# Optimization experiments

Measured on AMD Instinct MI355X. Metric: run time of the kernel, lower is better.

Reference implementation:

```python
import jax, jax.numpy as jnp
from jax import lax
import numpy as np

DIM = 384
H = W = 32
B = 32
HALF = DIM // 2


def _parc(x, pe, w, b, axis):
    """Global circular depthwise conv along `axis` (2=H, 3=W). w: (C,1,kh,kw)."""
    x = x + pe
    k = x.shape[axis]
    if axis == 2:
        x_cat = jnp.concatenate([x, x[:, :, : k - 1, :]], axis=2)
    else:
        x_cat = jnp.concatenate([x, x[:, :, :, : k - 1]], axis=3)
    out = lax.conv_general_dilated(
        x_cat, w, window_strides=(1, 1), padding='VALID',
        dimension_numbers=('NCHW', 'OIHW', 'NCHW'),
        feature_group_count=x.shape[1])
    return out + b[None, :, None, None]


def setup_inputs() -> dict:
    key = jax.random.key(0)
    ks = jax.random.split(key, 12)
    std = 0.02
    return {
        'x': jax.random.normal(ks[0], (B, DIM, H, W), jnp.float32),
        'pe_h': std * jax.random.normal(ks[1], (1, HALF, H, 1), jnp.float32),
        'w_h': std * jax.random.normal(ks[2], (HALF, 1, H, 1), jnp.float32),
        'b_h': jnp.zeros((HALF,), jnp.float32),
        'pe_w': std * jax.random.normal(ks[3], (1, HALF, 1, W), jnp.float32),
        'w_w': std * jax.random.normal(ks[4], (HALF, 1, 1, W), jnp.float32),
        'b_w': jnp.zeros((HALF,), jnp.float32),
        'ln_w': jnp.ones((DIM,), jnp.float32),
        'ln_b': jnp.zeros((DIM,), jnp.float32),
        'w1': std * jax.random.normal(ks[5], (DIM, 4 * DIM), jnp.float32),
        'b1': jnp.zeros((4 * DIM,), jnp.float32),
        'w2': std * jax.random.normal(ks[6], (4 * DIM, DIM), jnp.float32),
        'b2': jnp.zeros((DIM,), jnp.float32),
        'gamma': 1e-6 * jnp.ones((DIM,), jnp.float32),
    }


def reference(x, pe_h, w_h, b_h, pe_w, w_w, b_w, ln_w, ln_b, w1, b1, w2, b2, gamma):
    inp = x
    half = x.shape[1] // 2
    x_h = _parc(x[:, :half], pe_h, w_h, b_h, axis=2)
    x_w = _parc(x[:, half:], pe_w, w_w, b_w, axis=3)
    y = jnp.concatenate([x_h, x_w], axis=1).transpose(0, 2, 3, 1)  # NHWC
    # LayerNorm over channels (eps=1e-6)
    mu = y.mean(-1, keepdims=True)
    var = ((y - mu) ** 2).mean(-1, keepdims=True)
    y = (y - mu) / jnp.sqrt(var + 1e-6) * ln_w + ln_b
    # inverted MLP: dim -> 4*dim -> dim with exact GELU
    y = jax.nn.gelu(jnp.dot(y, w1) + b1, approximate=False)
    y = jnp.dot(y, w2) + b2
    y = gamma * y
    return inp + y.transpose(0, 3, 1, 2)
```

## Files before the change

### kernel.cpp

```cpp
#include <hip/hip_runtime.h>


typedef __attribute__((ext_vector_type(8))) short short8;
typedef __attribute__((ext_vector_type(4))) float f32x4;
typedef __attribute__((ext_vector_type(16))) float f32x16;
typedef __attribute__((ext_vector_type(4))) int int4v;
typedef __attribute__((ext_vector_type(8))) int i32x8;

__device__ __forceinline__ float bf2f(unsigned short u) {
  union { unsigned int i; float f; } v; v.i = ((unsigned int)u) << 16; return v.f;
}
__device__ __forceinline__ unsigned short f2bf(float f) {
  union { float f; unsigned int i; } v; v.f = f;
  unsigned int r = v.i + 0x7FFFu + ((v.i >> 16) & 1u);
  return (unsigned short)(r >> 16);
}

#if defined(__has_builtin)
#if __has_builtin(__builtin_amdgcn_global_load_lds)
#define HAS_GLL 1
#endif
#endif
#ifndef HAS_GLL
#define HAS_GLL 0
#endif

#if HAS_GLL
__device__ __forceinline__ void gload16(const void* g, void* l) {
  __builtin_amdgcn_global_load_lds((const __attribute__((address_space(1))) void*)g,
                                   (__attribute__((address_space(3))) void*)l, 16, 0, 0);
}
#else
__device__ __forceinline__ void gload16(const void* g, void* l) {
  *(f32x4*)l = *(const f32x4*)g;
}
#endif

template <int N>
__device__ __forceinline__ void wait_vm() {
  asm volatile("s_waitcnt vmcnt(%0)" :: "n"(N) : "memory");
}
__device__ __forceinline__ void barrier_raw() {
  __builtin_amdgcn_s_barrier();
  __builtin_amdgcn_sched_barrier(0);
}

__device__ __forceinline__ float fast_gelu(float h) {
  const float e = __builtin_amdgcn_exp2f(-2.4554005f * h);
  return h * __builtin_amdgcn_rcpf(1.f + e);
}

__device__ __forceinline__ int pk4(float a, float b, float c, float d) {
  int r = __builtin_amdgcn_cvt_pk_fp8_f32(a, b, 0, false);
  return __builtin_amdgcn_cvt_pk_fp8_f32(c, d, r, true);
}

#define SCL1 0x7F7F7F7F

__device__ __forceinline__ int packed_off(int row, int kc) {
  return ((row >> 5) << 11) + ((kc & 1) << 10) + ((kc >> 1) << 9) + ((row & 31) << 4);
}

__global__ __launch_bounds__(256) void pack_kernel(
    const float* __restrict__ w1, const float* __restrict__ w2,
    char* __restrict__ w1p, char* __restrict__ w2p) {
  const int t = threadIdx.x;
  const int bid = blockIdx.x;
  float v[64];
  if (bid < 36) {
    const int kt = bid % 6, hg = bid / 6;
    const int h = hg * 256 + t;
    #pragma unroll
    for (int k = 0; k < 64; ++k) v[k] = w1[(size_t)(kt * 64 + k) * 1536 + h];
    char* base = w1p + (size_t)kt * 1536 * 64;
    #pragma unroll
    for (int k0 = 0; k0 < 64; k0 += 4) {
      *(int*)(base + packed_off(h, k0 >> 4) + (k0 & 12)) =
          pk4(v[k0], v[k0 + 1], v[k0 + 2], v[k0 + 3]);
    }
  } else {
    const int kt = bid - 36;
    for (int c = t; c < 384; c += 256) {
      #pragma unroll
      for (int k = 0; k < 64; ++k) v[k] = w2[(size_t)(kt * 64 + k) * 384 + c];
      char* base = w2p + (size_t)kt * 384 * 64;
      #pragma unroll
      for (int k0 = 0; k0 < 64; k0 += 4) {
        *(int*)(base + packed_off(c, k0 >> 4) + (k0 & 12)) =
            pk4(v[k0], v[k0 + 1], v[k0 + 2], v[k0 + 3]);
      }
    }
  }
}

__global__ __launch_bounds__(256) void conv_kernel(
    const float* __restrict__ x,
    const float* __restrict__ pe_h, const float* __restrict__ w_h, const float* __restrict__ b_h,
    const float* __restrict__ pe_w, const float* __restrict__ w_w, const float* __restrict__ b_w,
    unsigned short* __restrict__ convout) {
  __shared__ float wt_s[8][32], pe_s[8][32], pc_s[8][32];
  const int t = threadIdx.x;
  const int bid = blockIdx.x;
  const int b = bid / 48, g = bid % 48;
  const int c0 = g << 3;
  const bool ish = (c0 < 192);
  const int cl = t >> 5, q = t & 31;
  {
    const int c = c0 + cl;
    if (ish) { wt_s[cl][q] = w_h[(c << 5) + q];           pe_s[cl][q] = pe_h[(c << 5) + q]; }
    else     { const int cc = c - 192;
               wt_s[cl][q] = w_w[(cc << 5) + q];          pe_s[cl][q] = pe_w[(cc << 5) + q]; }
  }
  __syncthreads();
  {
    float s = ish ? b_h[c0 + cl] : b_w[c0 + cl - 192];
    #pragma unroll
    for (int i = 0; i < 32; ++i) s += pe_s[cl][(q + i) & 31] * wt_s[cl][i];
    pc_s[cl][q] = s;
  }
  __syncthreads();
  const float* xp = x + ((size_t)(b * 384 + c0 + cl) << 10);
  float col[32];
  if (ish) {
    #pragma unroll
    for (int j = 0; j < 32; ++j) col[j] = xp[(j << 5) + q];
  } else {
    const float* rp = xp + (q << 5);
    #pragma unroll
    for (int j4 = 0; j4 < 8; ++j4) {
      f32x4 v = *(const f32x4*)&rp[j4 << 2];
      col[j4 * 4 + 0] = v[0]; col[j4 * 4 + 1] = v[1];
      col[j4 * 4 + 2] = v[2]; col[j4 * 4 + 3] = v[3];
    }
  }
  float wr[32];
  #pragma unroll
  for (int i = 0; i < 32; ++i) wr[i] = wt_s[cl][i];
  float o[32];
  #pragma unroll
  for (int oo = 0; oo < 32; ++oo) o[oo] = pc_s[cl][oo];
  #pragma unroll
  for (int i = 0; i < 32; ++i)
    #pragma unroll
    for (int oo = 0; oo < 32; ++oo)
      o[oo] = fmaf(col[(oo + i) & 31], wr[i], o[oo]);
  unsigned short* op = convout + ((size_t)(b * 384 + c0 + cl) << 10);
  if (ish) {
    #pragma unroll
    for (int oo = 0; oo < 32; ++oo) op[(oo << 5) + q] = f2bf(o[oo]);
  } else {
    #pragma unroll
    for (int j8 = 0; j8 < 4; ++j8) {
      short8 p;
      #pragma unroll
      for (int j = 0; j < 8; ++j) p[j] = (short)f2bf(o[j8 * 8 + j]);
      *(short8*)&op[(q << 5) + j8 * 8] = p;
    }
  }
}

__global__ __launch_bounds__(256) void ln_fused_kernel(
    const unsigned short* __restrict__ conv, char* __restrict__ ylnp,
    const float* __restrict__ ln_w, const float* __restrict__ ln_b) {
  __shared__ unsigned short tile[384][72];
  __shared__ float lws[384], lbs[384];
  __shared__ float ps[4][64], pq[4][64];
  __shared__ float mus[64], rss[64];
  const int t = threadIdx.x;
  const int pb = blockIdx.x;
  const int b = pb >> 4;
  const int hw0 = (pb & 15) << 6;
  for (int i = t; i < 384; i += 256) { lws[i] = ln_w[i]; lbs[i] = ln_b[i]; }
  #pragma unroll
  for (int i = 0; i < 12; ++i) {
    const int idx = t + i * 256;
    const int c = idx >> 3, j = idx & 7;
    short8 v = *(const short8*)(conv + (((size_t)(b * 384 + c)) << 10) + hw0 + j * 8);
    *(short8*)&tile[c][j * 8] = v;
  }
  __syncthreads();
  {
    const int l = t & 63, qt = t >> 6;
    float s = 0.f, ss = 0.f;
    #pragma unroll
    for (int k = 0; k < 96; ++k) {
      const float v = bf2f(tile[qt * 96 + k][l]);
      s += v; ss = fmaf(v, v, ss);
    }
    ps[qt][l] = s; pq[qt][l] = ss;
  }
  __syncthreads();
  if (t < 64) {
    const float st = ps[0][t] + ps[1][t] + ps[2][t] + ps[3][t];
    const float sq = pq[0][t] + pq[1][t] + pq[2][t] + pq[3][t];
    const float m = st * (1.f / 384.f);
    const float var = sq * (1.f / 384.f) - m * m;
    mus[t] = m; rss[t] = rsqrtf(var + 1e-6f);
  }
  __syncthreads();
  const int l = t & 63, kc = t >> 6;
  const int px = pb * 64 + l;
  const float m = mus[l], r = rss[l];
  #pragma unroll
  for (int kt = 0; kt < 6; ++kt) {
    const int c0 = kt * 64 + kc * 16;
    float ov[16];
    #pragma unroll
    for (int e = 0; e < 16; ++e) {
      const float v = bf2f(tile[c0 + e][l]);
      ov[e] = (v - m) * r * lws[c0 + e] + lbs[c0 + e];
    }
    int4v d;
    d[0] = pk4(ov[0],  ov[1],  ov[2],  ov[3]);
    d[1] = pk4(ov[4],  ov[5],  ov[6],  ov[7]);
    d[2] = pk4(ov[8],  ov[9],  ov[10], ov[11]);
    d[3] = pk4(ov[12], ov[13], ov[14], ov[15]);
    *(int4v*)(ylnp + (size_t)kt * 32768 * 64 + packed_off(px, kc)) = d;
  }
}

template <int EPI, int KDIM, int AROWS, int BN>
__global__ __launch_bounds__(512, 4) void gemm_kernel(
    const char* __restrict__ Ab, const char* __restrict__ Bb,
    char* __restrict__ Hout8, const float* __restrict__ bias,
    const float* __restrict__ gamma, const float* __restrict__ xres,
    float* __restrict__ out, int px0, int bstride, int boff, int hstride,
    int nwg, int nx) {
  extern __shared__ char lds[];
  constexpr int BM = 128;
  constexpr int FN = BN / 64;
  constexpr int NB = 3, DEPTH = 2;
  constexpr int NT = KDIM / 64;
  constexpr int SLOT = (BM + BN) * 64;
  constexpr int CH = (BM + BN) * 4 / 512;
  constexpr int BCH = BN * 4 / 512;
  const int tid = threadIdx.x;
  const int lane = tid & 63;
  const int wid = tid >> 6;
  const int wm = wid >> 1;
  const int wn = wid & 1;
  const int lane31 = lane & 31;
  const int kh = lane >> 5;
  const int bid = blockIdx.x;
  const int q = nwg >> 3, r = nwg & 7;
  const int xcd = bid & 7, idx = bid >> 3;
  const int lg = (xcd < r ? xcd * (q + 1) : r * (q + 1) + (xcd - r) * q) + idx;
  const int xb = lg % nx, yb = lg / nx;
  const int arow0 = xb * BM;
  const int brow0 = yb * BN;

  f32x16 acc[FN] = {};

  const int abase = (wm << 11) + (kh << 9) + (lane31 << 4);
  int bbase[FN];
  #pragma unroll
  for (int n = 0; n < FN; ++n)
    bbase[n] = BM * 64 + ((wn * FN + n) << 11) + (kh << 9) + (lane31 << 4);

  auto stage = [&](int tile) {
    char* sl = lds + (tile % NB) * SLOT;
    gload16(Ab + ((size_t)tile * AROWS + arow0) * 64 + tid * 16, sl + tid * 16);
    const char* bsrc = Bb + ((size_t)tile * bstride + boff + brow0) * 64;
    #pragma unroll
    for (int i = 0; i < BCH; ++i)
      gload16(bsrc + (i * 512 + tid) * 16, sl + BM * 64 + (i * 512 + tid) * 16);
  };

  auto step = [&](int t, int stage_tile) {
    const char* slp = lds + (t % NB) * SLOT;
    int4v a0 = *(const int4v*)(slp + abase);
    int4v a1 = *(const int4v*)(slp + abase + 1024);
    i32x8 av;
    av[0] = a0[0]; av[1] = a0[1]; av[2] = a0[2]; av[3] = a0[3];
    av[4] = a1[0]; av[5] = a1[1]; av[6] = a1[2]; av[7] = a1[3];
    i32x8 bv[FN];
    #pragma unroll
    for (int n = 0; n < FN; ++n) {
      int4v p0 = *(const int4v*)(slp + bbase[n]);
      int4v p1 = *(const int4v*)(slp + bbase[n] + 1024);
      bv[n][0] = p0[0]; bv[n][1] = p0[1]; bv[n][2] = p0[2]; bv[n][3] = p0[3];
      bv[n][4] = p1[0]; bv[n][5] = p1[1]; bv[n][6] = p1[2]; bv[n][7] = p1[3];
    }
    if (stage_tile >= 0) stage(stage_tile);
    __builtin_amdgcn_s_setprio(1);
    #pragma unroll
    for (int n = 0; n < FN; ++n)
      acc[n] = __builtin_amdgcn_mfma_scale_f32_32x32x64_f8f6f4(
          av, bv[n], acc[n], 0, 0, 0, SCL1, 0, SCL1);
    __builtin_amdgcn_s_setprio(0);
  };

  #pragma unroll
  for (int d = 0; d < DEPTH; ++d) stage(d);
  wait_vm<CH * (DEPTH - 1)>();
  barrier_raw();

  #pragma unroll 1
  for (int t = 0; t < NT - DEPTH; ++t) {
    step(t, t + DEPTH);
    wait_vm<CH * (DEPTH - 1)>();
    barrier_raw();
  }
  step(NT - 2, -1);
  wait_vm<0>();
  barrier_raw();
  step(NT - 1, -1);

  if (EPI == 0) {
    const int kt2 = (arow0 >> 6) + (wm >> 1);
    #pragma unroll
    for (int G = 0; G < 4; ++G) {
      const int hbyte = ((wm & 1) << 5) + 8 * G + 4 * kh;
      const int hglob = arow0 + (wm << 5) + 8 * G + 4 * kh;
      const float c0 = bias[hglob + 0], c1 = bias[hglob + 1];
      const float c2 = bias[hglob + 2], c3 = bias[hglob + 3];
      const int kc = hbyte >> 4, sub = hbyte & 15;
      #pragma unroll
      for (int n = 0; n < FN; ++n) {
        const int px = brow0 + (wn * FN + n) * 32 + lane31;
        const int d = pk4(fast_gelu(acc[n][4 * G + 0] + c0),
                          fast_gelu(acc[n][4 * G + 1] + c1),
                          fast_gelu(acc[n][4 * G + 2] + c2),
                          fast_gelu(acc[n][4 * G + 3] + c3));
        *(int*)(Hout8 + (size_t)kt2 * hstride * 64 + packed_off(px, kc) + sub) = d;
      }
    }
  } else {
    #pragma unroll
    for (int G = 0; G < 4; ++G) {
      #pragma unroll
      for (int j = 0; j < 4; ++j) {
        const int c = arow0 + (wm << 5) + 8 * G + 4 * kh + j;
        const float gv = gamma[c];
        const float bvv = bias[c];
        #pragma unroll
        for (int n = 0; n < FN; ++n) {
          const int px = px0 + brow0 + (wn * FN + n) * 32 + lane31;
          const int bb = px >> 10, hw = px & 1023;
          const size_t oi = (((size_t)(bb * 384 + c)) << 10) + hw;
          out[oi] = xres[oi] + gv * (acc[n][4 * G + j] + bvv);
        }
      }
    }
  }
}

extern "C" void kernel_launch(void* const* d_in, const int* in_sizes, int n_in,
                              void* d_out, int out_size, void* d_ws, size_t ws_size,
                              hipStream_t stream) {
  (void)in_sizes; (void)n_in; (void)out_size;
  const float* x     = (const float*)d_in[0];
  const float* pe_h  = (const float*)d_in[1];
  const float* w_h   = (const float*)d_in[2];
  const float* b_h   = (const float*)d_in[3];
  const float* pe_w  = (const float*)d_in[4];
  const float* w_w   = (const float*)d_in[5];
  const float* b_w   = (const float*)d_in[6];
  const float* ln_w  = (const float*)d_in[7];
  const float* ln_b  = (const float*)d_in[8];
  const float* w1    = (const float*)d_in[9];
  const float* b1    = (const float*)d_in[10];
  const float* w2    = (const float*)d_in[11];
  const float* b2    = (const float*)d_in[12];
  const float* gamma = (const float*)d_in[13];
  float* out = (float*)d_out;
  char* ws = (char*)d_ws;

  char*           W1P  = ws;
  char*           W2P  = ws + 589824;
  char*           YLNP = ws + 1441792;
  unsigned short* CONV = (unsigned short*)(ws + 14024704);
  char*           HID  = ws + 14024704;

  int G = 32;
  while (G > 2) {
    size_t hid = (size_t)G * 1572864ull;
    size_t need = 14024704ull + (hid > 25165824ull ? hid : 25165824ull);
    if (need <= ws_size) break;
    G -= 2;
  }

  constexpr int LDS1 = (128 + 256) * 64 * 3;
  constexpr int LDS2 = (128 + 128) * 64 * 3;
  (void)hipFuncSetAttribute((const void*)gemm_kernel<0, 384, 1536, 256>,
                            hipFuncAttributeMaxDynamicSharedMemorySize, LDS1);

  pack_kernel<<<dim3(60), dim3(256), 0, stream>>>(w1, w2, W1P, W2P);
  conv_kernel<<<dim3(1536), dim3(256), 0, stream>>>(x, pe_h, w_h, b_h, pe_w, w_w, b_w, CONV);
  ln_fused_kernel<<<dim3(512), dim3(256), 0, stream>>>(CONV, YLNP, ln_w, ln_b);
  for (int i0 = 0; i0 < 32; i0 += G) {
    const int gi = (32 - i0 < G) ? (32 - i0) : G;
    const int Mpx = gi * 1024;
    {
      const int nwg = 12 * (Mpx / 256);
      gemm_kernel<0, 384, 1536, 256><<<dim3(nwg), dim3(512), LDS1, stream>>>(
          W1P, YLNP, HID, b1, nullptr, nullptr, nullptr,
          0, 32768, i0 * 1024, Mpx, nwg, 12);
    }
    {
      const int nwg = 3 * (Mpx / 128);
      gemm_kernel<1, 1536, 384, 128><<<dim3(nwg), dim3(512), LDS2, stream>>>(
          W2P, HID, nullptr, b2, gamma, x, out, i0 * 1024, Mpx, 0, 0, nwg, 3);
    }
  }
}
```

Before: 104.8 us.

## Give each GEMM wave a 2x2 MFMA tile and resize workgroups

Each wave in the GEMM kernel now computes a 64x64 output block as a 2x2 grid of 32x32 MFMAs. Before, each wave held one 32-row A fragment and reused it across the N fragments. The block width comes from the number of N-waves, so the first GEMM keeps 512 threads and the second GEMM drops to 256 threads per workgroup. Each fragment loaded from LDS now feeds two MFMAs, which cuts LDS read traffic per MFMA, at the cost of more accumulator registers per wave and fewer waves in the second GEMM.

```diff
diff --git a/kernel.cpp b/kernel.cpp
--- a/kernel.cpp
+++ b/kernel.cpp
@@ -219,8 +219,8 @@
   }
 }
 
-template <int EPI, int KDIM, int AROWS, int BN>
-__global__ __launch_bounds__(512, 4) void gemm_kernel(
+template <int EPI, int KDIM, int AROWS, int NWN>
+__global__ __launch_bounds__(NWN * 128, 4) void gemm_kernel(
     const char* __restrict__ Ab, const char* __restrict__ Bb,
     char* __restrict__ Hout8, const float* __restrict__ bias,
     const float* __restrict__ gamma, const float* __restrict__ xres,
@@ -228,17 +228,19 @@
     int nwg, int nx) {
   extern __shared__ char lds[];
   constexpr int BM = 128;
-  constexpr int FN = BN / 64;
+  constexpr int BN = NWN * 64;
+  constexpr int THREADS = NWN * 128;
   constexpr int NB = 3, DEPTH = 2;
   constexpr int NT = KDIM / 64;
   constexpr int SLOT = (BM + BN) * 64;
-  constexpr int CH = (BM + BN) * 4 / 512;
-  constexpr int BCH = BN * 4 / 512;
+  constexpr int ACH = BM * 4 / THREADS;
+  constexpr int BCH = BN * 4 / THREADS;
+  constexpr int CH = ACH + BCH;
   const int tid = threadIdx.x;
   const int lane = tid & 63;
   const int wid = tid >> 6;
-  const int wm = wid >> 1;
-  const int wn = wid & 1;
+  const int wm = wid / NWN;
+  const int wn = wid % NWN;
   const int lane31 = lane & 31;
   const int kh = lane >> 5;
   const int bid = blockIdx.x;
@@ -249,33 +251,40 @@
   const int arow0 = xb * BM;
   const int brow0 = yb * BN;
 
-  f32x16 acc[FN] = {};
-
-  const int abase = (wm << 11) + (kh << 9) + (lane31 << 4);
-  int bbase[FN];
-  #pragma unroll
-  for (int n = 0; n < FN; ++n)
-    bbase[n] = BM * 64 + ((wn * FN + n) << 11) + (kh << 9) + (lane31 << 4);
+  f32x16 acc[2][2] = {};
+
+  int abase[2], bbase[2];
+  #pragma unroll
+  for (int fm = 0; fm < 2; ++fm)
+    abase[fm] = ((wm * 2 + fm) << 11) + (kh << 9) + (lane31 << 4);
+  #pragma unroll
+  for (int n = 0; n < 2; ++n)
+    bbase[n] = BM * 64 + ((wn * 2 + n) << 11) + (kh << 9) + (lane31 << 4);
 
   auto stage = [&](int tile) {
     char* sl = lds + (tile % NB) * SLOT;
-    gload16(Ab + ((size_t)tile * AROWS + arow0) * 64 + tid * 16, sl + tid * 16);
+    const char* asrc = Ab + ((size_t)tile * AROWS + arow0) * 64;
+    #pragma unroll
+    for (int i = 0; i < ACH; ++i)
+      gload16(asrc + (i * THREADS + tid) * 16, sl + (i * THREADS + tid) * 16);
     const char* bsrc = Bb + ((size_t)tile * bstride + boff + brow0) * 64;
     #pragma unroll
     for (int i = 0; i < BCH; ++i)
-      gload16(bsrc + (i * 512 + tid) * 16, sl + BM * 64 + (i * 512 + tid) * 16);
+      gload16(bsrc + (i * THREADS + tid) * 16, sl + BM * 64 + (i * THREADS + tid) * 16);
   };
 
   auto step = [&](int t, int stage_tile) {
     const char* slp = lds + (t % NB) * SLOT;
-    int4v a0 = *(const int4v*)(slp + abase);
-    int4v a1 = *(const int4v*)(slp + abase + 1024);
-    i32x8 av;
-    av[0] = a0[0]; av[1] = a0[1]; av[2] = a0[2]; av[3] = a0[3];
-    av[4] = a1[0]; av[5] = a1[1]; av[6] = a1[2]; av[7] = a1[3];
-    i32x8 bv[FN];
-    #pragma unroll
-    for (int n = 0; n < FN; ++n) {
+    i32x8 av[2], bv[2];
+    #pragma unroll
+    for (int fm = 0; fm < 2; ++fm) {
+      int4v p0 = *(const int4v*)(slp + abase[fm]);
+      int4v p1 = *(const int4v*)(slp + abase[fm] + 1024);
+      av[fm][0] = p0[0]; av[fm][1] = p0[1]; av[fm][2] = p0[2]; av[fm][3] = p0[3];
+      av[fm][4] = p1[0]; av[fm][5] = p1[1]; av[fm][6] = p1[2]; av[fm][7] = p1[3];
+    }
+    #pragma unroll
+    for (int n = 0; n < 2; ++n) {
       int4v p0 = *(const int4v*)(slp + bbase[n]);
       int4v p1 = *(const int4v*)(slp + bbase[n] + 1024);
       bv[n][0] = p0[0]; bv[n][1] = p0[1]; bv[n][2] = p0[2]; bv[n][3] = p0[3];
@@ -284,9 +293,11 @@
     if (stage_tile >= 0) stage(stage_tile);
     __builtin_amdgcn_s_setprio(1);
     #pragma unroll
-    for (int n = 0; n < FN; ++n)
-      acc[n] = __builtin_amdgcn_mfma_scale_f32_32x32x64_f8f6f4(
-          av, bv[n], acc[n], 0, 0, 0, SCL1, 0, SCL1);
+    for (int fm = 0; fm < 2; ++fm)
+      #pragma unroll
+      for (int n = 0; n < 2; ++n)
+        acc[fm][n] = __builtin_amdgcn_mfma_scale_f32_32x32x64_f8f6f4(
+            av[fm], bv[n], acc[fm][n], 0, 0, 0, SCL1, 0, SCL1);
     __builtin_amdgcn_s_setprio(0);
   };
 
@@ -307,38 +318,46 @@
   step(NT - 1, -1);
 
   if (EPI == 0) {
-    const int kt2 = (arow0 >> 6) + (wm >> 1);
-    #pragma unroll
-    for (int G = 0; G < 4; ++G) {
-      const int hbyte = ((wm & 1) << 5) + 8 * G + 4 * kh;
-      const int hglob = arow0 + (wm << 5) + 8 * G + 4 * kh;
-      const float c0 = bias[hglob + 0], c1 = bias[hglob + 1];
-      const float c2 = bias[hglob + 2], c3 = bias[hglob + 3];
-      const int kc = hbyte >> 4, sub = hbyte & 15;
-      #pragma unroll
-      for (int n = 0; n < FN; ++n) {
-        const int px = brow0 + (wn * FN + n) * 32 + lane31;
-        const int d = pk4(fast_gelu(acc[n][4 * G + 0] + c0),
-                          fast_gelu(acc[n][4 * G + 1] + c1),
-                          fast_gelu(acc[n][4 * G + 2] + c2),
-                          fast_gelu(acc[n][4 * G + 3] + c3));
-        *(int*)(Hout8 + (size_t)kt2 * hstride * 64 + packed_off(px, kc) + sub) = d;
+    #pragma unroll
+    for (int fm = 0; fm < 2; ++fm) {
+      const int wmf = wm * 2 + fm;
+      const int kt2 = (arow0 >> 6) + (wmf >> 1);
+      #pragma unroll
+      for (int G = 0; G < 4; ++G) {
+        const int hbyte = ((wmf & 1) << 5) + 8 * G + 4 * kh;
+        const int hglob = arow0 + (wmf << 5) + 8 * G + 4 * kh;
+        const float c0 = bias[hglob + 0], c1 = bias[hglob + 1];
+        const float c2 = bias[hglob + 2], c3 = bias[hglob + 3];
+        const int kc = hbyte >> 4, sub = hbyte & 15;
+        #pragma unroll
+        for (int n = 0; n < 2; ++n) {
+          const int px = brow0 + wn * 64 + n * 32 + lane31;
+          const int d = pk4(fast_gelu(acc[fm][n][4 * G + 0] + c0),
+                            fast_gelu(acc[fm][n][4 * G + 1] + c1),
+                            fast_gelu(acc[fm][n][4 * G + 2] + c2),
+                            fast_gelu(acc[fm][n][4 * G + 3] + c3));
+          *(int*)(Hout8 + (size_t)kt2 * hstride * 64 + packed_off(px, kc) + sub) = d;
+        }
       }
     }
   } else {
     #pragma unroll
-    for (int G = 0; G < 4; ++G) {
-      #pragma unroll
-      for (int j = 0; j < 4; ++j) {
-        const int c = arow0 + (wm << 5) + 8 * G + 4 * kh + j;
-        const float gv = gamma[c];
-        const float bvv = bias[c];
+    for (int fm = 0; fm < 2; ++fm) {
+      const int wmf = wm * 2 + fm;
+      #pragma unroll
+      for (int G = 0; G < 4; ++G) {
         #pragma unroll
-        for (int n = 0; n < FN; ++n) {
-          const int px = px0 + brow0 + (wn * FN + n) * 32 + lane31;
-          const int bb = px >> 10, hw = px & 1023;
-          const size_t oi = (((size_t)(bb * 384 + c)) << 10) + hw;
-          out[oi] = xres[oi] + gv * (acc[n][4 * G + j] + bvv);
+        for (int j = 0; j < 4; ++j) {
+          const int c = arow0 + (wmf << 5) + 8 * G + 4 * kh + j;
+          const float gv = gamma[c];
+          const float bvv = bias[c];
+          #pragma unroll
+          for (int n = 0; n < 2; ++n) {
+            const int px = px0 + brow0 + wn * 64 + n * 32 + lane31;
+            const int bb = px >> 10, hw = px & 1023;
+            const size_t oi = (((size_t)(bb * 384 + c)) << 10) + hw;
+            out[oi] = xres[oi] + gv * (acc[fm][n][4 * G + j] + bvv);
+          }
         }
       }
     }
@@ -382,7 +401,7 @@
 
   constexpr int LDS1 = (128 + 256) * 64 * 3;
   constexpr int LDS2 = (128 + 128) * 64 * 3;
-  (void)hipFuncSetAttribute((const void*)gemm_kernel<0, 384, 1536, 256>,
+  (void)hipFuncSetAttribute((const void*)gemm_kernel<0, 384, 1536, 4>,
                             hipFuncAttributeMaxDynamicSharedMemorySize, LDS1);
 
   pack_kernel<<<dim3(60), dim3(256), 0, stream>>>(w1, w2, W1P, W2P);
@@ -393,13 +412,13 @@
     const int Mpx = gi * 1024;
     {
       const int nwg = 12 * (Mpx / 256);
-      gemm_kernel<0, 384, 1536, 256><<<dim3(nwg), dim3(512), LDS1, stream>>>(
+      gemm_kernel<0, 384, 1536, 4><<<dim3(nwg), dim3(512), LDS1, stream>>>(
           W1P, YLNP, HID, b1, nullptr, nullptr, nullptr,
           0, 32768, i0 * 1024, Mpx, nwg, 12);
     }
     {
       const int nwg = 3 * (Mpx / 128);
-      gemm_kernel<1, 1536, 384, 128><<<dim3(nwg), dim3(512), LDS2, stream>>>(
+      gemm_kernel<1, 1536, 384, 2><<<dim3(nwg), dim3(256), LDS2, stream>>>(
           W2P, HID, nullptr, b2, gamma, x, out, i0 * 1024, Mpx, 0, 0, nwg, 3);
     }
   }
```

Result: faster. 100.3 us (-4.4%).
